# Performance work log

Measured on AMD Instinct MI355X. Metric: run time of the kernel, lower is better.

Reference implementation:

```python
import jax, jax.numpy as jnp
import numpy as np

EPS = 1e-7  # K.epsilon()


def setup_inputs() -> dict:
    key = jax.random.key(0)
    k1, k2, k3 = jax.random.split(key, 3)
    B, T, D = 32, 2048, 1024
    one = jax.random.normal(k1, (B, D), dtype=jnp.float32)
    many = jax.random.normal(k2, (B, T, D), dtype=jnp.float32)
    W = jax.random.normal(k3, (D, D), dtype=jnp.float32) * (1.0 / np.sqrt(D))
    return {"one": one, "many": many, "W": W}


def reference(one, many, W):
    # logits = batch_dot(tanh(many @ W), one, axes=[2,1]) -> [B, T]
    proj = jnp.tanh(jnp.einsum('btd,de->bte', many, W))       # [B,T,D]
    logits = jnp.einsum('btd,bd->bt', proj, one)               # [B,T]
    # stable softmax with Keras epsilon in denominator
    ai = jnp.exp(logits - jnp.max(logits, axis=-1, keepdims=True))
    att_weights = ai / (jnp.sum(ai, axis=-1, keepdims=True) + EPS)  # [B,T]
    result = jnp.einsum('btd,bt->bd', many, att_weights)       # [B,D]
    return result, att_weights
```

## Files before the change

### kernel.cpp

```cpp
#include <hip/hip_runtime.h>
#include <hip/hip_bf16.h>

typedef _Float16 half8v __attribute__((ext_vector_type(8)));
typedef __fp16  fp16x2 __attribute__((ext_vector_type(2)));
typedef float floatx4 __attribute__((ext_vector_type(4)));

#define NB 32
#define NT 2048
#define ND 1024
#define NM (NB * NT)

#define GL16(g, l)                                                             \
    __builtin_amdgcn_global_load_lds(                                          \
        (const __attribute__((address_space(1))) void*)(g),                    \
        (__attribute__((address_space(3))) void*)(l), 16, 0, 0)

__device__ __forceinline__ float fast_tanh(float x) {
    x = fminf(9.0f, fmaxf(-9.0f, x));
    float e = __builtin_amdgcn_exp2f(x * 2.8853900817779268f);
    return (e - 1.0f) * __builtin_amdgcn_rcpf(e + 1.0f);
}

__global__ __launch_bounds__(256)
void wt_kernel(const float* __restrict__ W, _Float16* __restrict__ Wt) {
    __shared__ float tile[32][33];
    int tx = threadIdx.x, ty = threadIdx.y;
    int bx = blockIdx.x, by = blockIdx.y;
    #pragma unroll
    for (int i = 0; i < 4; ++i) {
        int y = by * 32 + ty + i * 8;
        tile[ty + i * 8][tx] = W[y * ND + bx * 32 + tx];
    }
    __syncthreads();
    #pragma unroll
    for (int i = 0; i < 4; ++i) {
        int e = bx * 32 + ty + i * 8;
        Wt[e * ND + by * 32 + tx] = (_Float16)tile[tx][ty + i * 8];
    }
}

__global__ __launch_bounds__(256)
void conv_kernel(const float* __restrict__ many, _Float16* __restrict__ manyh) {
    size_t idx = ((size_t)blockIdx.x * 256 + threadIdx.x) * 8;
    size_t stride = (size_t)gridDim.x * 256 * 8;
    for (size_t i = idx; i < (size_t)NM * ND; i += stride) {
        float4 a = *reinterpret_cast<const float4*>(many + i);
        float4 b = *reinterpret_cast<const float4*>(many + i + 4);
        union { _Float16 h[8]; uint4 u; } o;
        o.h[0] = (_Float16)a.x; o.h[1] = (_Float16)a.y;
        o.h[2] = (_Float16)a.z; o.h[3] = (_Float16)a.w;
        o.h[4] = (_Float16)b.x; o.h[5] = (_Float16)b.y;
        o.h[6] = (_Float16)b.z; o.h[7] = (_Float16)b.w;
        *reinterpret_cast<uint4*>(manyh + i) = o.u;
    }
}

__global__ __launch_bounds__(512, 2)
void gemm_logits_8p(const _Float16* __restrict__ manyh, const _Float16* __restrict__ Wt,
                    const float* __restrict__ one, float* __restrict__ logits) {
    __shared__ uint4 LDSQ[8192];
    char* Ld = (char*)LDSQ;

    int bid = blockIdx.x;
    int j = (bid & 7) * 128 + (bid >> 3);
    int mb = j >> 2, nb = j & 3;
    int m0 = mb * 256, n0 = nb * 256;

    int tid = threadIdx.x;
    int lane = tid & 63, w = tid >> 6;
    int wr = w >> 2, wc = w & 3;
    int l15 = lane & 15, l4 = lane >> 4;

    const char* aS = (const char*)manyh + ((size_t)(m0 + (tid >> 2)) << 11)
                   + (size_t)(((tid & 3) ^ ((tid >> 3) & 3)) << 4);
    const char* bS = (const char*)Wt   + ((size_t)(n0 + (tid >> 2)) << 11)
                   + (size_t)(((tid & 3) ^ ((tid >> 3) & 3)) << 4);

#define STAGE2(QBASE, TP) do {                                                 \
        int nxt_ = ((TP) & 3) * 32768;                                         \
        int kn_ = (TP) * 64;                                                   \
        const char* s_ = (QBASE) < 2 ? aS : bS;                                \
        GL16(s_ + kn_,          Ld + nxt_ + (QBASE) * 8192 + tid * 16);        \
        GL16(s_ + 262144 + kn_, Ld + nxt_ + (QBASE) * 8192 + 8192 + tid * 16); \
    } while (0)

    floatx4 acc[8][4] = {};

    #pragma unroll
    for (int pre = 0; pre < 3; ++pre) { STAGE2(0, pre); STAGE2(2, pre); }
    asm volatile("s_waitcnt vmcnt(8)" ::: "memory");
    __builtin_amdgcn_sched_barrier(0);
    __builtin_amdgcn_s_barrier();

    #pragma unroll 1
    for (int t = 0; t < 32; ++t) {
        int cur = (t & 3) * 32768;
        half8v af[4], bf[4];
        #pragma unroll
        for (int mi = 0; mi < 4; ++mi) {
            int r = wr * 128 + mi * 16 + l15;
            af[mi] = *(const half8v*)(Ld + cur + r * 64 + ((l4 ^ ((r >> 1) & 3)) << 4));
        }
        #pragma unroll
        for (int ni = 0; ni < 4; ++ni) {
            int r = wc * 64 + ni * 16 + l15;
            bf[ni] = *(const half8v*)(Ld + cur + 16384 + r * 64 + ((l4 ^ ((r >> 1) & 3)) << 4));
        }
        if (t < 29) STAGE2(0, t + 3);
        __builtin_amdgcn_s_barrier();
        __builtin_amdgcn_s_setprio(1);
        #pragma unroll
        for (int mi = 0; mi < 4; ++mi)
            #pragma unroll
            for (int ni = 0; ni < 4; ++ni)
                acc[mi][ni] = __builtin_amdgcn_mfma_f32_16x16x32_f16(
                    af[mi], bf[ni], acc[mi][ni], 0, 0, 0);
        __builtin_amdgcn_s_setprio(0);
        __builtin_amdgcn_s_barrier();
        #pragma unroll
        for (int mi = 0; mi < 4; ++mi) {
            int r = wr * 128 + 64 + mi * 16 + l15;
            af[mi] = *(const half8v*)(Ld + cur + r * 64 + ((l4 ^ ((r >> 1) & 3)) << 4));
        }
        if (t < 29) STAGE2(2, t + 3);
        __builtin_amdgcn_s_barrier();
        __builtin_amdgcn_s_setprio(1);
        #pragma unroll
        for (int mi = 0; mi < 4; ++mi)
            #pragma unroll
            for (int ni = 0; ni < 4; ++ni)
                acc[4 + mi][ni] = __builtin_amdgcn_mfma_f32_16x16x32_f16(
                    af[mi], bf[ni], acc[4 + mi][ni], 0, 0, 0);
        __builtin_amdgcn_s_setprio(0);
        if (t <= 28)      asm volatile("s_waitcnt vmcnt(8)" ::: "memory");
        else if (t == 29) asm volatile("s_waitcnt vmcnt(4)" ::: "memory");
        else if (t == 30) asm volatile("s_waitcnt vmcnt(0)" ::: "memory");
        __builtin_amdgcn_sched_barrier(0);
        __builtin_amdgcn_s_barrier();
    }
#undef STAGE2

    int bidx = m0 >> 11;
    float onev[4];
    #pragma unroll
    for (int ni = 0; ni < 4; ++ni)
        onev[ni] = one[(bidx << 10) + n0 + wc * 64 + ni * 16 + l15];

    #pragma unroll
    for (int mi = 0; mi < 8; ++mi) {
        float part[4] = {0.f, 0.f, 0.f, 0.f};
        #pragma unroll
        for (int ni = 0; ni < 4; ++ni)
            #pragma unroll
            for (int b = 0; b < 4; ++b)
                part[b] += fast_tanh(acc[mi][ni][b]) * onev[ni];
        #pragma unroll
        for (int off = 1; off < 16; off <<= 1)
            #pragma unroll
            for (int b = 0; b < 4; ++b)
                part[b] += __shfl_xor(part[b], off, 64);
        #pragma unroll
        for (int b = 0; b < 4; ++b)
            if (l15 == ((mi * 4 + b) & 15))
                atomicAdd(&logits[m0 + wr * 128 + mi * 16 + l4 * 4 + b], part[b]);
    }
}

__global__ __launch_bounds__(256, 2)
void gemm_logits(const float* __restrict__ many, const _Float16* __restrict__ Wt,
                 const float* __restrict__ one, float* __restrict__ logits) {
    __shared__ uint4 AsQ[2048];
    __shared__ uint4 BsQ[1024];
    char* AsB = (char*)AsQ;
    char* BsB = (char*)BsQ;

    int bid = blockIdx.x;
    int j = (bid & 7) * 512 + (bid >> 3);
    int mb = j >> 3, nb = j & 7;
    int m0 = mb * 128, n0 = nb * 128;

    int tid = threadIdx.x;
    int lane = tid & 63, w = tid >> 6;
    int wr = w >> 1, wc = w & 1;
    int l15 = lane & 15, l4 = lane >> 4;

    const char* aS = (const char*)many + ((size_t)(m0 + (tid >> 4)) << 12)
        + (size_t)(((tid & 15) ^ ((tid >> 4) & 7)) << 4);
    const char* bS = (const char*)Wt + ((size_t)(n0 + (tid >> 3)) << 11)
        + (size_t)(((tid & 7) ^ ((tid >> 3) & 7)) << 4);
    char* aD = AsB + tid * 16;
    char* bD = BsB + tid * 16;

    floatx4 acc[4][4] = {};

    for (int kb = 0; kb < 1024; kb += 64) {
        #pragma unroll
        for (int i = 0; i < 8; ++i)
            GL16(aS + kb * 4 + i * 65536, aD + i * 4096);
        #pragma unroll
        for (int i = 0; i < 4; ++i)
            GL16(bS + kb * 2 + i * 65536, bD + i * 4096);
        __syncthreads();

        #pragma unroll
        for (int ks = 0; ks < 64; ks += 32) {
            half8v af[4], bf[4];
            #pragma unroll
            for (int mi = 0; mi < 4; ++mi) {
                int r = wr * 64 + mi * 16 + l15;
                int s = l15 & 7;
                const char* base = AsB + r * 256;
                int c0 = (ks >> 2) + l4 * 2;
                float4 x = *(const float4*)(base + (size_t)((c0 ^ s) << 4));
                float4 y = *(const float4*)(base + (size_t)(((c0 + 1) ^ s) << 4));
                union { fp16x2 p[4]; half8v h; } u;
                u.p[0] = __builtin_amdgcn_cvt_pkrtz(x.x, x.y);
                u.p[1] = __builtin_amdgcn_cvt_pkrtz(x.z, x.w);
                u.p[2] = __builtin_amdgcn_cvt_pkrtz(y.x, y.y);
                u.p[3] = __builtin_amdgcn_cvt_pkrtz(y.z, y.w);
                af[mi] = u.h;
            }
            #pragma unroll
            for (int ni = 0; ni < 4; ++ni) {
                int r = wc * 64 + ni * 16 + l15;
                int s = l15 & 7;
                int c = (ks >> 3) + l4;
                bf[ni] = *(const half8v*)(BsB + r * 128 + (size_t)((c ^ s) << 4));
            }
            #pragma unroll
            for (int mi = 0; mi < 4; ++mi)
                #pragma unroll
                for (int ni = 0; ni < 4; ++ni)
                    acc[mi][ni] = __builtin_amdgcn_mfma_f32_16x16x32_f16(
                        af[mi], bf[ni], acc[mi][ni], 0, 0, 0);
        }
        __syncthreads();
    }

    int bidx = m0 >> 11;
    float onev[4];
    #pragma unroll
    for (int ni = 0; ni < 4; ++ni)
        onev[ni] = one[(bidx << 10) + n0 + wc * 64 + ni * 16 + l15];

    #pragma unroll
    for (int mi = 0; mi < 4; ++mi) {
        float part[4] = {0.f, 0.f, 0.f, 0.f};
        #pragma unroll
        for (int ni = 0; ni < 4; ++ni)
            #pragma unroll
            for (int b = 0; b < 4; ++b)
                part[b] += fast_tanh(acc[mi][ni][b]) * onev[ni];
        #pragma unroll
        for (int off = 1; off < 16; off <<= 1)
            #pragma unroll
            for (int b = 0; b < 4; ++b)
                part[b] += __shfl_xor(part[b], off, 64);
        #pragma unroll
        for (int b = 0; b < 4; ++b)
            if (l15 == mi * 4 + b)
                atomicAdd(&logits[m0 + wr * 64 + mi * 16 + l4 * 4 + b], part[b]);
    }
}

__global__ __launch_bounds__(256)
void softmax_kernel(const float* __restrict__ logits, float* __restrict__ att) {
    int b = blockIdx.x, tid = threadIdx.x;
    const float* lr = logits + (b << 11);
    float lv[8];
    float mx = -1e30f;
    #pragma unroll
    for (int i = 0; i < 8; ++i) { lv[i] = lr[tid + (i << 8)]; mx = fmaxf(mx, lv[i]); }
    #pragma unroll
    for (int off = 1; off < 64; off <<= 1) mx = fmaxf(mx, __shfl_xor(mx, off, 64));
    __shared__ float redm[4];
    __shared__ float reds[4];
    int wv = tid >> 6;
    if ((tid & 63) == 0) redm[wv] = mx;
    __syncthreads();
    mx = fmaxf(fmaxf(redm[0], redm[1]), fmaxf(redm[2], redm[3]));
    float s = 0.f;
    #pragma unroll
    for (int i = 0; i < 8; ++i) { lv[i] = expf(lv[i] - mx); s += lv[i]; }
    #pragma unroll
    for (int off = 1; off < 64; off <<= 1) s += __shfl_xor(s, off, 64);
    if ((tid & 63) == 0) reds[wv] = s;
    __syncthreads();
    s = reds[0] + reds[1] + reds[2] + reds[3];
    float inv = 1.0f / (s + 1e-7f);
    #pragma unroll
    for (int i = 0; i < 8; ++i) att[(b << 11) + tid + (i << 8)] = lv[i] * inv;
}

__global__ __launch_bounds__(256)
void out_kernel_h(const _Float16* __restrict__ manyh, const float* __restrict__ att,
                  float* __restrict__ out) {
    int b = blockIdx.x >> 4, tch = blockIdx.x & 15;
    int tid = threadIdx.x;
    __shared__ float aw[128];
    if (tid < 128) aw[tid] = att[(b << 11) + tch * 128 + tid];
    __syncthreads();
    const _Float16* mp = manyh + (((size_t)b * NT + tch * 128) << 10) + tid * 4;
    float a0 = 0.f, a1 = 0.f, a2 = 0.f, a3 = 0.f;
    for (int t = 0; t < 128; ++t) {
        float wgt = aw[t];
        union { _Float16 h[4]; uint2 u; } v;
        v.u = *reinterpret_cast<const uint2*>(mp + ((size_t)t << 10));
        a0 = fmaf((float)v.h[0], wgt, a0); a1 = fmaf((float)v.h[1], wgt, a1);
        a2 = fmaf((float)v.h[2], wgt, a2); a3 = fmaf((float)v.h[3], wgt, a3);
    }
    float* op = out + (b << 10) + tid * 4;
    atomicAdd(op + 0, a0); atomicAdd(op + 1, a1);
    atomicAdd(op + 2, a2); atomicAdd(op + 3, a3);
}

__global__ __launch_bounds__(256)
void out_kernel(const float* __restrict__ many, const float* __restrict__ att,
                float* __restrict__ out) {
    int b = blockIdx.x >> 4, tch = blockIdx.x & 15;
    int tid = threadIdx.x;
    __shared__ float aw[128];
    if (tid < 128) aw[tid] = att[(b << 11) + tch * 128 + tid];
    __syncthreads();
    const float* mp = many + (((size_t)b * NT + tch * 128) << 10) + tid * 4;
    float ax = 0.f, ay = 0.f, az = 0.f, aww = 0.f;
    for (int t = 0; t < 128; ++t) {
        float wgt = aw[t];
        float4 v = *reinterpret_cast<const float4*>(mp + ((size_t)t << 10));
        ax = fmaf(v.x, wgt, ax); ay = fmaf(v.y, wgt, ay);
        az = fmaf(v.z, wgt, az); aww = fmaf(v.w, wgt, aww);
    }
    float* op = out + (b << 10) + tid * 4;
    atomicAdd(op + 0, ax); atomicAdd(op + 1, ay);
    atomicAdd(op + 2, az); atomicAdd(op + 3, aww);
}

extern "C" void kernel_launch(void* const* d_in, const int* in_sizes, int n_in,
                              void* d_out, int out_size, void* d_ws, size_t ws_size,
                              hipStream_t stream) {
    const float* one  = (const float*)d_in[0];
    const float* many = (const float*)d_in[1];
    const float* W    = (const float*)d_in[2];
    float* out = (float*)d_out;

    size_t wtB = (size_t)ND * ND * 2;
    size_t lgB = (size_t)NM * 4;
    size_t mhB = (size_t)NM * ND * 2;
    _Float16* Wt    = (_Float16*)d_ws;
    float*    logits = (float*)((char*)d_ws + wtB);
    _Float16* manyh = (_Float16*)((char*)d_ws + wtB + lgB);
    float*    att   = out + NB * ND;
    bool big = ws_size >= wtB + lgB + mhB;

    (void)hipMemsetAsync(out, 0, (size_t)NB * ND * sizeof(float), stream);
    (void)hipMemsetAsync(logits, 0, (size_t)NM * sizeof(float), stream);

    wt_kernel<<<dim3(32, 32), dim3(32, 8), 0, stream>>>(W, Wt);
    if (big) {
        conv_kernel<<<2048, 256, 0, stream>>>(many, manyh);
        gemm_logits_8p<<<1024, 512, 0, stream>>>(manyh, Wt, one, logits);
    } else {
        gemm_logits<<<4096, 256, 0, stream>>>(many, Wt, one, logits);
    }
    softmax_kernel<<<NB, 256, 0, stream>>>(logits, att);
    if (big) out_kernel_h<<<NB * 16, 256, 0, stream>>>(manyh, att, out);
    else     out_kernel<<<NB * 16, 256, 0, stream>>>(many, att, out);
}
```

Before: 279.5 us.

## Restructure GEMM main loop to BK=128 double-buffered with finer-grained staging

The logits GEMM main loop now processes K in 128-wide tiles over 16 iterations with two LDS buffers, instead of 64-wide tiles over 32 iterations with a four-deep ring. Global-to-LDS loads are split into eight sub-chunks interleaved across four MFMA phases per iteration, and the XOR swizzle is widened to eight 16-byte columns. The aim is to halve loop and barrier overhead per FLOP and to spread memory issue more evenly between MFMA bursts. In exchange, prefetch depth drops and each iteration has more barriers.

```diff
diff --git a/kernel.cpp b/kernel.cpp
--- a/kernel.cpp
+++ b/kernel.cpp
@@ -71,74 +71,79 @@
     int wr = w >> 2, wc = w & 3;
     int l15 = lane & 15, l4 = lane >> 4;
 
-    const char* aS = (const char*)manyh + ((size_t)(m0 + (tid >> 2)) << 11)
-                   + (size_t)(((tid & 3) ^ ((tid >> 3) & 3)) << 4);
-    const char* bS = (const char*)Wt   + ((size_t)(n0 + (tid >> 2)) << 11)
-                   + (size_t)(((tid & 3) ^ ((tid >> 3) & 3)) << 4);
-
-#define STAGE2(QBASE, TP) do {                                                 \
-        int nxt_ = ((TP) & 3) * 32768;                                         \
-        int kn_ = (TP) * 64;                                                   \
-        const char* s_ = (QBASE) < 2 ? aS : bS;                                \
-        GL16(s_ + kn_,          Ld + nxt_ + (QBASE) * 8192 + tid * 16);        \
-        GL16(s_ + 262144 + kn_, Ld + nxt_ + (QBASE) * 8192 + 8192 + tid * 16); \
-    } while (0)
+    const char* aS = (const char*)manyh + ((size_t)(m0 + (tid >> 3)) << 11)
+                   + (size_t)(((tid & 7) ^ ((tid >> 3) & 7)) << 4);
+    const char* bS = (const char*)Wt + ((size_t)(n0 + (tid >> 3)) << 11)
+                   + (size_t)(((tid & 7) ^ ((tid >> 3) & 7)) << 4);
+    int ldst = tid * 16;
+
+#define SU(OP, H, L, TT)                                                        \
+    GL16(((OP) ? bS : aS) + (((size_t)((H) * 128 + (L) * 64)) << 11) + (TT) * 128, \
+         Ld + (((TT) & 1) << 16) + ((OP) << 15) + ((H) << 14) + ((L) << 13) + ldst)
 
     floatx4 acc[8][4] = {};
-
-    #pragma unroll
-    for (int pre = 0; pre < 3; ++pre) { STAGE2(0, pre); STAGE2(2, pre); }
-    asm volatile("s_waitcnt vmcnt(8)" ::: "memory");
+    int key = l15 & 7;
+    int lofA0 = l15 * 128 + (((0 | l4) ^ key) << 4);
+    int lofA1 = l15 * 128 + (((4 | l4) ^ key) << 4);
+
+    SU(0, 0, 0, 0); SU(0, 1, 0, 0);
+    SU(0, 0, 1, 0); SU(0, 1, 1, 0);
+    SU(1, 0, 0, 0); SU(1, 0, 1, 0);
+    SU(1, 1, 0, 0); SU(1, 1, 1, 0);
+    SU(0, 0, 0, 1); SU(0, 1, 0, 1);
+    asm volatile("s_waitcnt vmcnt(2)" ::: "memory");
     __builtin_amdgcn_sched_barrier(0);
     __builtin_amdgcn_s_barrier();
 
     #pragma unroll 1
-    for (int t = 0; t < 32; ++t) {
-        int cur = (t & 3) * 32768;
-        half8v af[4], bf[4];
-        #pragma unroll
-        for (int mi = 0; mi < 4; ++mi) {
-            int r = wr * 128 + mi * 16 + l15;
-            af[mi] = *(const half8v*)(Ld + cur + r * 64 + ((l4 ^ ((r >> 1) & 3)) << 4));
+    for (int t = 0; t < 16; ++t) {
+        const char* ab = Ld + ((t & 1) << 16) + (wr << 14);
+        const char* bb = Ld + ((t & 1) << 16) + 32768 + ((wc >> 1) << 14)
+                       + ((wc & 1) << 13);
+        half8v bf0[4], bf1[4];
+        #pragma unroll
+        for (int p = 0; p < 4; ++p) {
+            int rb = (p * 32) << 7;
+            half8v a0k0 = *(const half8v*)(ab + rb + lofA0);
+            half8v a0k1 = *(const half8v*)(ab + rb + lofA1);
+            half8v a1k0 = *(const half8v*)(ab + rb + (16 << 7) + lofA0);
+            half8v a1k1 = *(const half8v*)(ab + rb + (16 << 7) + lofA1);
+            if (p == 0) {
+                #pragma unroll
+                for (int ni = 0; ni < 4; ++ni) {
+                    bf0[ni] = *(const half8v*)(bb + ((ni * 16) << 7) + lofA0);
+                    bf1[ni] = *(const half8v*)(bb + ((ni * 16) << 7) + lofA1);
+                }
+            }
+            if (t < 15) {
+                if (p == 0)      { SU(0, 0, 1, t + 1); SU(0, 1, 1, t + 1); }
+                else if (p == 1) { SU(1, 0, 0, t + 1); SU(1, 0, 1, t + 1); }
+                else if (p == 2) { SU(1, 1, 0, t + 1); SU(1, 1, 1, t + 1); }
+                else if (t < 14) { SU(0, 0, 0, t + 2); SU(0, 1, 0, t + 2); }
+            }
+            __builtin_amdgcn_s_barrier();
+            __builtin_amdgcn_s_setprio(1);
+            #pragma unroll
+            for (int ni = 0; ni < 4; ++ni) {
+                acc[2 * p][ni] = __builtin_amdgcn_mfma_f32_16x16x32_f16(
+                    a0k0, bf0[ni], acc[2 * p][ni], 0, 0, 0);
+                acc[2 * p][ni] = __builtin_amdgcn_mfma_f32_16x16x32_f16(
+                    a0k1, bf1[ni], acc[2 * p][ni], 0, 0, 0);
+                acc[2 * p + 1][ni] = __builtin_amdgcn_mfma_f32_16x16x32_f16(
+                    a1k0, bf0[ni], acc[2 * p + 1][ni], 0, 0, 0);
+                acc[2 * p + 1][ni] = __builtin_amdgcn_mfma_f32_16x16x32_f16(
+                    a1k1, bf1[ni], acc[2 * p + 1][ni], 0, 0, 0);
+            }
+            __builtin_amdgcn_s_setprio(0);
+            if (p == 3) {
+                if (t < 14)       asm volatile("s_waitcnt vmcnt(2)" ::: "memory");
+                else if (t == 14) asm volatile("s_waitcnt vmcnt(0)" ::: "memory");
+                __builtin_amdgcn_sched_barrier(0);
+            }
+            __builtin_amdgcn_s_barrier();
         }
-        #pragma unroll
-        for (int ni = 0; ni < 4; ++ni) {
-            int r = wc * 64 + ni * 16 + l15;
-            bf[ni] = *(const half8v*)(Ld + cur + 16384 + r * 64 + ((l4 ^ ((r >> 1) & 3)) << 4));
-        }
-        if (t < 29) STAGE2(0, t + 3);
-        __builtin_amdgcn_s_barrier();
-        __builtin_amdgcn_s_setprio(1);
-        #pragma unroll
-        for (int mi = 0; mi < 4; ++mi)
-            #pragma unroll
-            for (int ni = 0; ni < 4; ++ni)
-                acc[mi][ni] = __builtin_amdgcn_mfma_f32_16x16x32_f16(
-                    af[mi], bf[ni], acc[mi][ni], 0, 0, 0);
-        __builtin_amdgcn_s_setprio(0);
-        __builtin_amdgcn_s_barrier();
-        #pragma unroll
-        for (int mi = 0; mi < 4; ++mi) {
-            int r = wr * 128 + 64 + mi * 16 + l15;
-            af[mi] = *(const half8v*)(Ld + cur + r * 64 + ((l4 ^ ((r >> 1) & 3)) << 4));
-        }
-        if (t < 29) STAGE2(2, t + 3);
-        __builtin_amdgcn_s_barrier();
-        __builtin_amdgcn_s_setprio(1);
-        #pragma unroll
-        for (int mi = 0; mi < 4; ++mi)
-            #pragma unroll
-            for (int ni = 0; ni < 4; ++ni)
-                acc[4 + mi][ni] = __builtin_amdgcn_mfma_f32_16x16x32_f16(
-                    af[mi], bf[ni], acc[4 + mi][ni], 0, 0, 0);
-        __builtin_amdgcn_s_setprio(0);
-        if (t <= 28)      asm volatile("s_waitcnt vmcnt(8)" ::: "memory");
-        else if (t == 29) asm volatile("s_waitcnt vmcnt(4)" ::: "memory");
-        else if (t == 30) asm volatile("s_waitcnt vmcnt(0)" ::: "memory");
-        __builtin_amdgcn_sched_barrier(0);
-        __builtin_amdgcn_s_barrier();
-    }
-#undef STAGE2
+    }
+#undef SU
 
     int bidx = m0 >> 11;
     float onev[4];
```

Result: faster. 272.8 us (-2.4%).

## Replace pipelined 256x256 fp16 GEMM with simpler 128x128 single-buffered tile kernel

Applied to the files above, without the earlier changes.

Swaps the 512-thread, 256x256-tile GEMM with a 4-deep global-to-LDS prefetch ring for a 256-thread, 128x128-tile kernel. The new kernel loads each 64-wide K slice and synchronizes before computing, with an XOR-swizzled 128-byte-row LDS layout. It is meant to cut LDS use and register pressure so more blocks fit per CU and hide latency through occupancy. In exchange it loses explicit load/compute overlap and halves operand reuse per tile, which raises global and LDS traffic.

```diff
diff --git a/kernel.cpp b/kernel.cpp
--- a/kernel.cpp
+++ b/kernel.cpp
@@ -55,90 +55,63 @@
     }
 }
 
-__global__ __launch_bounds__(512, 2)
-void gemm_logits_8p(const _Float16* __restrict__ manyh, const _Float16* __restrict__ Wt,
-                    const float* __restrict__ one, float* __restrict__ logits) {
-    __shared__ uint4 LDSQ[8192];
+__global__ __launch_bounds__(256, 4)
+void gemm_logits_s(const _Float16* __restrict__ manyh, const _Float16* __restrict__ Wt,
+                   const float* __restrict__ one, float* __restrict__ logits) {
+    __shared__ uint4 LDSQ[2048];
     char* Ld = (char*)LDSQ;
 
     int bid = blockIdx.x;
-    int j = (bid & 7) * 128 + (bid >> 3);
-    int mb = j >> 2, nb = j & 3;
-    int m0 = mb * 256, n0 = nb * 256;
+    int j = (bid & 7) * 512 + (bid >> 3);
+    int mb = j >> 3, nb = j & 7;
+    int m0 = mb * 128, n0 = nb * 128;
 
     int tid = threadIdx.x;
     int lane = tid & 63, w = tid >> 6;
-    int wr = w >> 2, wc = w & 3;
+    int wr = w >> 1, wc = w & 1;
     int l15 = lane & 15, l4 = lane >> 4;
 
-    const char* aS = (const char*)manyh + ((size_t)(m0 + (tid >> 2)) << 11)
-                   + (size_t)(((tid & 3) ^ ((tid >> 3) & 3)) << 4);
-    const char* bS = (const char*)Wt   + ((size_t)(n0 + (tid >> 2)) << 11)
-                   + (size_t)(((tid & 3) ^ ((tid >> 3) & 3)) << 4);
-
-#define STAGE2(QBASE, TP) do {                                                 \
-        int nxt_ = ((TP) & 3) * 32768;                                         \
-        int kn_ = (TP) * 64;                                                   \
-        const char* s_ = (QBASE) < 2 ? aS : bS;                                \
-        GL16(s_ + kn_,          Ld + nxt_ + (QBASE) * 8192 + tid * 16);        \
-        GL16(s_ + 262144 + kn_, Ld + nxt_ + (QBASE) * 8192 + 8192 + tid * 16); \
-    } while (0)
-
-    floatx4 acc[8][4] = {};
-
-    #pragma unroll
-    for (int pre = 0; pre < 3; ++pre) { STAGE2(0, pre); STAGE2(2, pre); }
-    asm volatile("s_waitcnt vmcnt(8)" ::: "memory");
-    __builtin_amdgcn_sched_barrier(0);
-    __builtin_amdgcn_s_barrier();
+    const char* aS = (const char*)manyh + ((size_t)(m0 + (tid >> 3)) << 11)
+                   + (size_t)(((tid & 7) ^ ((tid >> 3) & 7)) << 4);
+    const char* bS = (const char*)Wt + ((size_t)(n0 + (tid >> 3)) << 11)
+                   + (size_t)(((tid & 7) ^ ((tid >> 3) & 7)) << 4);
+
+    floatx4 acc[4][4] = {};
 
     #pragma unroll 1
-    for (int t = 0; t < 32; ++t) {
-        int cur = (t & 3) * 32768;
-        half8v af[4], bf[4];
-        #pragma unroll
-        for (int mi = 0; mi < 4; ++mi) {
-            int r = wr * 128 + mi * 16 + l15;
-            af[mi] = *(const half8v*)(Ld + cur + r * 64 + ((l4 ^ ((r >> 1) & 3)) << 4));
+    for (int kb = 0; kb < 1024; kb += 64) {
+        #pragma unroll
+        for (int i = 0; i < 4; ++i)
+            GL16(aS + kb * 2 + i * 65536, Ld + i * 4096 + tid * 16);
+        #pragma unroll
+        for (int i = 0; i < 4; ++i)
+            GL16(bS + kb * 2 + i * 65536, Ld + 16384 + i * 4096 + tid * 16);
+        __syncthreads();
+
+        #pragma unroll
+        for (int ks = 0; ks < 64; ks += 32) {
+            half8v af[4], bf[4];
+            #pragma unroll
+            for (int mi = 0; mi < 4; ++mi) {
+                int r = wr * 64 + mi * 16 + l15;
+                int c = (ks >> 3) + l4;
+                af[mi] = *(const half8v*)(Ld + r * 128 + ((c ^ (r & 7)) << 4));
+            }
+            #pragma unroll
+            for (int ni = 0; ni < 4; ++ni) {
+                int r = wc * 64 + ni * 16 + l15;
+                int c = (ks >> 3) + l4;
+                bf[ni] = *(const half8v*)(Ld + 16384 + r * 128 + ((c ^ (r & 7)) << 4));
+            }
+            #pragma unroll
+            for (int mi = 0; mi < 4; ++mi)
+                #pragma unroll
+                for (int ni = 0; ni < 4; ++ni)
+                    acc[mi][ni] = __builtin_amdgcn_mfma_f32_16x16x32_f16(
+                        af[mi], bf[ni], acc[mi][ni], 0, 0, 0);
         }
-        #pragma unroll
-        for (int ni = 0; ni < 4; ++ni) {
-            int r = wc * 64 + ni * 16 + l15;
-            bf[ni] = *(const half8v*)(Ld + cur + 16384 + r * 64 + ((l4 ^ ((r >> 1) & 3)) << 4));
-        }
-        if (t < 29) STAGE2(0, t + 3);
-        __builtin_amdgcn_s_barrier();
-        __builtin_amdgcn_s_setprio(1);
-        #pragma unroll
-        for (int mi = 0; mi < 4; ++mi)
-            #pragma unroll
-            for (int ni = 0; ni < 4; ++ni)
-                acc[mi][ni] = __builtin_amdgcn_mfma_f32_16x16x32_f16(
-                    af[mi], bf[ni], acc[mi][ni], 0, 0, 0);
-        __builtin_amdgcn_s_setprio(0);
-        __builtin_amdgcn_s_barrier();
-        #pragma unroll
-        for (int mi = 0; mi < 4; ++mi) {
-            int r = wr * 128 + 64 + mi * 16 + l15;
-            af[mi] = *(const half8v*)(Ld + cur + r * 64 + ((l4 ^ ((r >> 1) & 3)) << 4));
-        }
-        if (t < 29) STAGE2(2, t + 3);
-        __builtin_amdgcn_s_barrier();
-        __builtin_amdgcn_s_setprio(1);
-        #pragma unroll
-        for (int mi = 0; mi < 4; ++mi)
-            #pragma unroll
-            for (int ni = 0; ni < 4; ++ni)
-                acc[4 + mi][ni] = __builtin_amdgcn_mfma_f32_16x16x32_f16(
-                    af[mi], bf[ni], acc[4 + mi][ni], 0, 0, 0);
-        __builtin_amdgcn_s_setprio(0);
-        if (t <= 28)      asm volatile("s_waitcnt vmcnt(8)" ::: "memory");
-        else if (t == 29) asm volatile("s_waitcnt vmcnt(4)" ::: "memory");
-        else if (t == 30) asm volatile("s_waitcnt vmcnt(0)" ::: "memory");
-        __builtin_amdgcn_sched_barrier(0);
-        __builtin_amdgcn_s_barrier();
-    }
-#undef STAGE2
+        __syncthreads();
+    }
 
     int bidx = m0 >> 11;
     float onev[4];
@@ -147,7 +120,7 @@
         onev[ni] = one[(bidx << 10) + n0 + wc * 64 + ni * 16 + l15];
 
     #pragma unroll
-    for (int mi = 0; mi < 8; ++mi) {
+    for (int mi = 0; mi < 4; ++mi) {
         float part[4] = {0.f, 0.f, 0.f, 0.f};
         #pragma unroll
         for (int ni = 0; ni < 4; ++ni)
@@ -161,8 +134,8 @@
                 part[b] += __shfl_xor(part[b], off, 64);
         #pragma unroll
         for (int b = 0; b < 4; ++b)
-            if (l15 == ((mi * 4 + b) & 15))
-                atomicAdd(&logits[m0 + wr * 128 + mi * 16 + l4 * 4 + b], part[b]);
+            if (l15 == mi * 4 + b)
+                atomicAdd(&logits[m0 + wr * 64 + mi * 16 + l4 * 4 + b], part[b]);
     }
 }
 
@@ -358,7 +331,7 @@
     wt_kernel<<<dim3(32, 32), dim3(32, 8), 0, stream>>>(W, Wt);
     if (big) {
         conv_kernel<<<2048, 256, 0, stream>>>(many, manyh);
-        gemm_logits_8p<<<1024, 512, 0, stream>>>(manyh, Wt, one, logits);
+        gemm_logits_s<<<4096, 256, 0, stream>>>(manyh, Wt, one, logits);
     } else {
         gemm_logits<<<4096, 256, 0, stream>>>(many, Wt, one, logits);
     }
```

New measurement: 250.3 us. 10.4% less time.
